# Kernel optimization log

Hardware: AMD Instinct MI355X
Metric: run time of the kernel (lower is better)

## Reference

```python
import jax, jax.numpy as jnp
import numpy as np

K = 64  # number of salient positions

def setup_inputs() -> dict:
    key = jax.random.key(0)
    x = jax.random.normal(key, (16, 64, 256, 256), dtype=jnp.float32)
    return {"x": x}

def reference(x) -> jnp.ndarray:
    B, C, H, W = x.shape
    # [B, N, C] with N = H*W
    xf = x.reshape(B, C, H * W).transpose(0, 2, 1)
    # squared-L2 norm per position: [B, N]
    x_powsum = jnp.sum(xf * xf, axis=2)
    # top-k over N (largest, sorted)
    _, idx = jax.lax.top_k(x_powsum, K)          # [B, K]
    # gather selected rows: [B, K, C]
    out = jnp.take_along_axis(xf, idx[:, :, None], axis=1)
    return out
```

## Files before the change

### kernel.cpp

```cpp
#include <hip/hip_runtime.h>
#include <stdint.h>

#define B 16
#define C 64
#define N 65536
#define K 64

#define NBINS 8192
#define CAP   4096


__global__ __launch_bounds__(256) void powsum_hist_kernel(const float* __restrict__ x,
                                                          float* __restrict__ ps,
                                                          uint32_t* __restrict__ ghist) {
    __shared__ uint32_t lh[NBINS];
    const int b   = blockIdx.x >> 6;
    const int blk = blockIdx.x & 63;
    const int n4  = blk * 1024 + threadIdx.x * 4;

    for (int j = threadIdx.x; j < NBINS; j += 256) lh[j] = 0u;
    __syncthreads();

    const float4* xp = (const float4*)(x + (size_t)b * C * N + n4);
    float4 acc = {0.f, 0.f, 0.f, 0.f};
    #pragma unroll 8
    for (int c = 0; c < C; ++c) {
        float4 v = xp[(size_t)c * (N / 4)];
        acc.x += v.x * v.x;
        acc.y += v.y * v.y;
        acc.z += v.z * v.z;
        acc.w += v.w * v.w;
    }
    *(float4*)(ps + (size_t)b * N + n4) = acc;

    const uint4 ub = *(const uint4*)&acc;
    atomicAdd(&lh[ub.x >> 19], 1u);
    atomicAdd(&lh[ub.y >> 19], 1u);
    atomicAdd(&lh[ub.z >> 19], 1u);
    atomicAdd(&lh[ub.w >> 19], 1u);
    __syncthreads();

    uint32_t* gh = ghist + (size_t)b * NBINS;
    for (int j = threadIdx.x; j < NBINS; j += 256) {
        uint32_t c = lh[j];
        if (c) atomicAdd(&gh[j], c);
    }
}

__global__ __launch_bounds__(1024) void select_kernel(const float* __restrict__ x,
                                                      const float* __restrict__ ps,
                                                      const uint32_t* __restrict__ ghist,
                                                      float* __restrict__ out) {
    const int b   = blockIdx.x;
    const int tid = threadIdx.x;

    __shared__ uint32_t csum[1024];
    __shared__ uint32_t sh_binT;
    __shared__ uint32_t cand_v[CAP], cand_i[CAP];
    __shared__ uint32_t cnt;
    __shared__ uint32_t sel[K];

    const uint32_t* gh = ghist + (size_t)b * NBINS;
    uint32_t h[8];
    #pragma unroll
    for (int j = 0; j < 8; ++j) h[j] = gh[tid * 8 + j];
    uint32_t s = 0;
    #pragma unroll
    for (int j = 0; j < 8; ++j) s += h[j];
    csum[tid] = s;
    __syncthreads();
    for (int off = 1; off < 1024; off <<= 1) {
        uint32_t v = csum[tid] + ((tid + off < 1024) ? csum[tid + off] : 0u);
        __syncthreads();
        csum[tid] = v;
        __syncthreads();
    }
    const uint32_t nxt = (tid < 1023) ? csum[tid + 1] : 0u;
    uint32_t ls[9];
    ls[8] = nxt;
    #pragma unroll
    for (int j = 7; j >= 0; --j) ls[j] = ls[j + 1] + h[j];
    #pragma unroll
    for (int j = 0; j < 8; ++j) {
        if (ls[j] >= K && ls[j + 1] < K) sh_binT = (uint32_t)(tid * 8 + j);
    }
    if (tid == 0) cnt = 0u;
    __syncthreads();
    const uint32_t binT = sh_binT;

    const uint32_t* bits = (const uint32_t*)(ps + (size_t)b * N);
    for (int i = tid; i < N; i += 1024) {
        uint32_t v = bits[i];
        if ((v >> 19) >= binT) {
            uint32_t p = atomicAdd(&cnt, 1u);
            if (p < CAP) { cand_v[p] = v; cand_i[p] = (uint32_t)i; }
        }
    }
    __syncthreads();
    const uint32_t M = (cnt < (uint32_t)CAP) ? cnt : (uint32_t)CAP;

    for (uint32_t t = tid; t < M; t += 1024) {
        const uint32_t v = cand_v[t], id = cand_i[t];
        uint32_t r = 0;
        for (uint32_t j = 0; j < M; ++j) {
            const uint32_t vj = cand_v[j], ij = cand_i[j];
            r += (vj > v || (vj == v && ij < id)) ? 1u : 0u;
        }
        if (r < K) sel[r] = id;
    }
    __syncthreads();

    const int c = tid & 63;
    for (int k = tid >> 6; k < K; k += 16) {
        const uint32_t n = sel[k];
        out[((size_t)b * K + k) * C + c] = x[((size_t)b * C + c) * N + n];
    }
}

extern "C" void kernel_launch(void* const* d_in, const int* in_sizes, int n_in,
                              void* d_out, int out_size, void* d_ws, size_t ws_size,
                              hipStream_t stream) {
    const float* x   = (const float*)d_in[0];
    float*       out = (float*)d_out;
    float*       ps  = (float*)d_ws;
    uint32_t*    ghist = (uint32_t*)((char*)d_ws + (size_t)B * N * sizeof(float));

    hipMemsetAsync(ghist, 0, (size_t)B * NBINS * sizeof(uint32_t), stream);
    powsum_hist_kernel<<<dim3(B * 64), dim3(256), 0, stream>>>(x, ps, ghist);
    select_kernel<<<dim3(B), dim3(1024), 0, stream>>>(x, ps, ghist, out);
}
```

Measured before the change: 87.17 us.

## Split candidate selection into a grid-wide collect kernel and a per-batch sort kernel

The single-block-per-batch select kernel is split in two. A collect kernel runs 64 blocks per batch, and each block recomputes the histogram threshold and filters its slice of power sums into global candidate buffers through a global atomic counter. A small sort/gather kernel then ranks the candidates per batch and gathers the output rows. The histogram is also halved to 4096 bins, which is enough because non-negative float bits shifted by 19 stay below 4096. This removes the serial 65536-element scan done by only 16 blocks, at the cost of an extra launch, redundant prefix scans in every block, and global atomics.

```diff
diff --git a/kernel.cpp b/kernel.cpp
--- a/kernel.cpp
+++ b/kernel.cpp
@@ -6,9 +6,14 @@
 #define N 65536
 #define K 64
 
-#define NBINS 8192
+#define NBINS 4096
 #define CAP   4096
 
+#define PS_OFF    0
+#define GH_OFF    ((size_t)B * N * sizeof(float))
+#define CNT_OFF   (GH_OFF + (size_t)B * NBINS * sizeof(uint32_t))
+#define CV_OFF    (CNT_OFF + 256)
+#define CI_OFF    (CV_OFF + (size_t)B * CAP * sizeof(uint32_t))
 
 __global__ __launch_bounds__(256) void powsum_hist_kernel(const float* __restrict__ x,
                                                           float* __restrict__ ps,
@@ -47,63 +52,87 @@
     }
 }
 
-__global__ __launch_bounds__(1024) void select_kernel(const float* __restrict__ x,
-                                                      const float* __restrict__ ps,
+__global__ __launch_bounds__(256) void collect_kernel(const float* __restrict__ ps,
                                                       const uint32_t* __restrict__ ghist,
-                                                      float* __restrict__ out) {
-    const int b   = blockIdx.x;
+                                                      uint32_t* __restrict__ cnt,
+                                                      uint32_t* __restrict__ cand_v,
+                                                      uint32_t* __restrict__ cand_i) {
+    const int b   = blockIdx.x >> 6;
+    const int blk = blockIdx.x & 63;
     const int tid = threadIdx.x;
 
-    __shared__ uint32_t csum[1024];
+    __shared__ uint32_t csum[256];
     __shared__ uint32_t sh_binT;
-    __shared__ uint32_t cand_v[CAP], cand_i[CAP];
-    __shared__ uint32_t cnt;
-    __shared__ uint32_t sel[K];
 
     const uint32_t* gh = ghist + (size_t)b * NBINS;
-    uint32_t h[8];
+    uint32_t h[16];
+    const uint4* gh4 = (const uint4*)(gh + tid * 16);
     #pragma unroll
-    for (int j = 0; j < 8; ++j) h[j] = gh[tid * 8 + j];
+    for (int j = 0; j < 4; ++j) {
+        uint4 t4 = gh4[j];
+        h[4*j] = t4.x; h[4*j+1] = t4.y; h[4*j+2] = t4.z; h[4*j+3] = t4.w;
+    }
     uint32_t s = 0;
     #pragma unroll
-    for (int j = 0; j < 8; ++j) s += h[j];
+    for (int j = 0; j < 16; ++j) s += h[j];
     csum[tid] = s;
     __syncthreads();
-    for (int off = 1; off < 1024; off <<= 1) {
-        uint32_t v = csum[tid] + ((tid + off < 1024) ? csum[tid + off] : 0u);
+    for (int off = 1; off < 256; off <<= 1) {
+        uint32_t v = csum[tid] + ((tid + off < 256) ? csum[tid + off] : 0u);
         __syncthreads();
         csum[tid] = v;
         __syncthreads();
     }
-    const uint32_t nxt = (tid < 1023) ? csum[tid + 1] : 0u;
-    uint32_t ls[9];
-    ls[8] = nxt;
+    uint32_t ls[17];
+    ls[16] = (tid < 255) ? csum[tid + 1] : 0u;
     #pragma unroll
-    for (int j = 7; j >= 0; --j) ls[j] = ls[j + 1] + h[j];
+    for (int j = 15; j >= 0; --j) ls[j] = ls[j + 1] + h[j];
     #pragma unroll
-    for (int j = 0; j < 8; ++j) {
-        if (ls[j] >= K && ls[j + 1] < K) sh_binT = (uint32_t)(tid * 8 + j);
+    for (int j = 0; j < 16; ++j) {
+        if (ls[j] >= K && ls[j + 1] < K) sh_binT = (uint32_t)(tid * 16 + j);
     }
-    if (tid == 0) cnt = 0u;
     __syncthreads();
     const uint32_t binT = sh_binT;
 
+    const int n4 = blk * 1024 + tid * 4;
     const uint32_t* bits = (const uint32_t*)(ps + (size_t)b * N);
-    for (int i = tid; i < N; i += 1024) {
-        uint32_t v = bits[i];
-        if ((v >> 19) >= binT) {
-            uint32_t p = atomicAdd(&cnt, 1u);
-            if (p < CAP) { cand_v[p] = v; cand_i[p] = (uint32_t)i; }
+    uint4 v4 = *(const uint4*)(bits + n4);
+    uint32_t vv[4] = {v4.x, v4.y, v4.z, v4.w};
+    #pragma unroll
+    for (int j = 0; j < 4; ++j) {
+        if ((vv[j] >> 19) >= binT) {
+            uint32_t p = atomicAdd(&cnt[b], 1u);
+            if (p < CAP) {
+                cand_v[(size_t)b * CAP + p] = vv[j];
+                cand_i[(size_t)b * CAP + p] = (uint32_t)(n4 + j);
+            }
         }
     }
+}
+
+__global__ __launch_bounds__(256) void sort_gather_kernel(const float* __restrict__ x,
+                                                          const uint32_t* __restrict__ cnt,
+                                                          const uint32_t* __restrict__ cand_v,
+                                                          const uint32_t* __restrict__ cand_i,
+                                                          float* __restrict__ out) {
+    const int b   = blockIdx.x;
+    const int tid = threadIdx.x;
+
+    __shared__ uint32_t sv[CAP], si[CAP];
+    __shared__ uint32_t sel[K];
+
+    const uint32_t M = (cnt[b] < (uint32_t)CAP) ? cnt[b] : (uint32_t)CAP;
+    for (uint32_t t = tid; t < M; t += 256) {
+        sv[t] = cand_v[(size_t)b * CAP + t];
+        si[t] = cand_i[(size_t)b * CAP + t];
+    }
     __syncthreads();
-    const uint32_t M = (cnt < (uint32_t)CAP) ? cnt : (uint32_t)CAP;
 
-    for (uint32_t t = tid; t < M; t += 1024) {
-        const uint32_t v = cand_v[t], id = cand_i[t];
+    for (uint32_t t = tid; t < M; t += 256) {
+        const uint32_t v = sv[t], id = si[t];
         uint32_t r = 0;
         for (uint32_t j = 0; j < M; ++j) {
-            const uint32_t vj = cand_v[j], ij = cand_i[j];
+            const uint32_t vj = sv[j], ij = si[j];
             r += (vj > v || (vj == v && ij < id)) ? 1u : 0u;
         }
         if (r < K) sel[r] = id;
@@ -111,7 +140,7 @@
     __syncthreads();
 
     const int c = tid & 63;
-    for (int k = tid >> 6; k < K; k += 16) {
+    for (int k = tid >> 6; k < K; k += 4) {
         const uint32_t n = sel[k];
         out[((size_t)b * K + k) * C + c] = x[((size_t)b * C + c) * N + n];
     }
@@ -122,10 +151,16 @@
                               hipStream_t stream) {
     const float* x   = (const float*)d_in[0];
     float*       out = (float*)d_out;
-    float*       ps  = (float*)d_ws;
-    uint32_t*    ghist = (uint32_t*)((char*)d_ws + (size_t)B * N * sizeof(float));
+    char*        ws  = (char*)d_ws;
 
-    hipMemsetAsync(ghist, 0, (size_t)B * NBINS * sizeof(uint32_t), stream);
+    float*    ps     = (float*)(ws + PS_OFF);
+    uint32_t* ghist  = (uint32_t*)(ws + GH_OFF);
+    uint32_t* cnt    = (uint32_t*)(ws + CNT_OFF);
+    uint32_t* cand_v = (uint32_t*)(ws + CV_OFF);
+    uint32_t* cand_i = (uint32_t*)(ws + CI_OFF);
+
+    hipMemsetAsync(ghist, 0, (CNT_OFF - GH_OFF) + 256, stream);
     powsum_hist_kernel<<<dim3(B * 64), dim3(256), 0, stream>>>(x, ps, ghist);
-    select_kernel<<<dim3(B), dim3(1024), 0, stream>>>(x, ps, ghist, out);
+    collect_kernel<<<dim3(B * 64), dim3(256), 0, stream>>>(ps, ghist, cnt, cand_v, cand_i);
+    sort_gather_kernel<<<dim3(B), dim3(256), 0, stream>>>(x, cnt, cand_v, cand_i, out);
 }
```

Result: faster. 80.66 us (-7.5%).
